# Kernel optimization log

Measured on AMD Instinct MI355X. Metric: run time of the kernel, lower is better.

The kernel has to match this reference:

```python
import jax, jax.numpy as jnp
import numpy as np

DIM = 768; NH = 8; G = 14; N = G * G + 1; B = 64; PD = DIM // 16; HID = 4 * DIM
SCOPES = (1, 4, 7)


def _build_adj(fs, scope):
    # windowed adjacency on an fs x fs grid, padded with an always-on ACM (class) token
    idx = np.arange(fs)
    ii, jj = np.meshgrid(idx, idx, indexing='ij')
    ri, rj = ii.ravel(), jj.ravel()
    a = ((np.abs(ri[:, None] - ri[None, :]) <= scope) & (np.abs(rj[:, None] - rj[None, :]) <= scope)).astype(np.float32)
    out = np.ones((fs * fs + 1, fs * fs + 1), np.float32)
    out[1:, 1:] = a
    return out


def _prior_adj():
    # loop=0 -> loop1=loop2=0, repeat = NH//4; heads get [adj1,adj1,adj2,adj2,adj3,adj3,ones,ones]
    rep = NH // 4
    mats = [_build_adj(G, s) for s in SCOPES] + [np.ones((N, N), np.float32)]
    return np.stack([m for m in mats for _ in range(rep)], 0)


def _rel_idx():
    coords = np.stack(np.meshgrid(np.arange(G), np.arange(G), indexing='ij')).reshape(2, -1)
    rel = (coords[:, :, None] - coords[:, None, :]).transpose(1, 2, 0).copy()
    rel[..., 0] += G - 1
    rel[..., 1] += G - 1
    rel[..., 0] *= 2 * G - 1
    idx = rel.sum(-1)
    out = np.full((N, N), (2 * G - 1) ** 2 + 1, np.int32)
    out[1:, 1:] = idx
    return out


def _biases():
    r = np.arange(-G, G + 1)  # arange(1-(G+1), G+1)
    g = np.stack(np.meshgrid(r, r, indexing='ij')).reshape(2, -1).T
    return g.astype(np.float32)  # ((2G+1)^2, 2)


def setup_inputs():
    key = jax.random.key(0)
    ks = iter(jax.random.split(key, 32))
    rn = lambda *s: jax.random.normal(next(ks), s, jnp.float32) * 0.02
    return dict(
        x=jax.random.normal(next(ks), (B, N, DIM), jnp.float32),
        norm1_w=jnp.ones(DIM), norm1_b=jnp.zeros(DIM),
        qkv_w=rn(3 * DIM, DIM),
        scale=10.0 * jnp.ones((NH, 1, 1)),
        pp_w=rn(PD, 2), pp_b=jnp.zeros(PD),
        ln1_w=jnp.ones(PD), ln1_b=jnp.zeros(PD), fcp1_w=rn(PD, PD), fcp1_b=jnp.zeros(PD),
        ln2_w=jnp.ones(PD), ln2_b=jnp.zeros(PD), fcp2_w=rn(PD, PD), fcp2_b=jnp.zeros(PD),
        ln3_w=jnp.ones(PD), ln3_b=jnp.zeros(PD), fcp3_w=rn(NH, PD), fcp3_b=jnp.zeros(NH),
        pre_w=rn(NH, NH) + jnp.eye(NH), post_w=rn(NH, NH) + jnp.eye(NH),
        proj_w=rn(DIM, DIM), proj_b=jnp.zeros(DIM),
        norm2_w=jnp.ones(DIM), norm2_b=jnp.zeros(DIM),
        m1_w=rn(HID, DIM), m1_b=jnp.zeros(HID),
        m2_w=rn(DIM, HID), m2_b=jnp.zeros(DIM),
        prior_adj=jnp.asarray(_prior_adj()),
        biases=jnp.asarray(_biases()),
        rel_idx=jnp.asarray(_rel_idx()),
    )


def _ln(x, w, b, eps=1e-5):
    m = x.mean(-1, keepdims=True)
    v = ((x - m) ** 2).mean(-1, keepdims=True)
    return (x - m) / jnp.sqrt(v + eps) * w + b


def _l2n(x, eps=1e-12):
    return x / jnp.maximum(jnp.linalg.norm(x, axis=-1, keepdims=True), eps)


def reference(x, norm1_w, norm1_b, qkv_w, scale, pp_w, pp_b, ln1_w, ln1_b, fcp1_w, fcp1_b, ln2_w, ln2_b, fcp2_w, fcp2_b, ln3_w, ln3_b, fcp3_w, fcp3_b, pre_w, post_w, proj_w, proj_b, norm2_w, norm2_b, m1_w, m1_b, m2_w, m2_b, prior_adj, biases, rel_idx):
    Bq, Nq, C = x.shape
    d = C // NH
    h = _ln(x, norm1_w, norm1_b)
    qkv = (h @ qkv_w.T).reshape(Bq, Nq, 3, NH, d).transpose(2, 0, 3, 1, 4)
    q, k, v = qkv[0], qkv[1], qkv[2]  # each (B, NH, N, d)
    attn = jnp.einsum('bhnd,bhmd->bhnm', _l2n(q), _l2n(k)) * jnp.minimum(scale, 100.0)[None]
    p = biases @ pp_w.T + pp_b
    p = jax.nn.relu(_ln(p, ln1_w, ln1_b)) @ fcp1_w.T + fcp1_b
    p = jax.nn.relu(_ln(p, ln2_w, ln2_b)) @ fcp2_w.T + fcp2_b
    p = jax.nn.relu(_ln(p, ln3_w, ln3_b)) @ fcp3_w.T + fcp3_b  # (841, NH)
    rpb = p[rel_idx]  # (N, N, NH)
    attn = attn + rpb.transpose(2, 0, 1)[None]
    attn = jnp.einsum('oh,bhnm->bonm', pre_w, attn)  # 1x1 conv over heads (pre-softmax)
    attn = jnp.where(prior_adj[None] > 0, attn, -1e9)
    attn = jax.nn.softmax(attn, axis=-1)
    attn = jnp.einsum('oh,bhnm->bonm', post_w, attn)  # 1x1 conv over heads (post-softmax)
    out = jnp.einsum('bhnm,bhmd->bhnd', attn, v).transpose(0, 2, 1, 3).reshape(Bq, Nq, C)
    x = x + (out @ proj_w.T + proj_b)
    h2 = _ln(x, norm2_w, norm2_b)
    h2 = jax.nn.gelu(h2 @ m1_w.T + m1_b, approximate=False) @ m2_w.T + m2_b
    return x + h2
```

## Files before the change

kernel.cpp:

```cpp
#include <hip/hip_runtime.h>
#include <hip/hip_bf16.h>
#include <math.h>

typedef __hip_bfloat16 bf16;
typedef __attribute__((ext_vector_type(8))) short bf16x8;
typedef __attribute__((ext_vector_type(4))) float f32x4;

__device__ __forceinline__ float b2f(bf16 x){ return __bfloat162float(x); }
__device__ __forceinline__ bf16  f2b(float x){ return __float2bfloat16(x); }

__device__ __forceinline__ void gld16(const bf16* g, bf16* l){
    __builtin_amdgcn_global_load_lds(
        (const __attribute__((address_space(1))) unsigned int*)g,
        (__attribute__((address_space(3))) unsigned int*)l, 16, 0, 0);
}

#define NTOK 197
#define NBATCH 64
#define NHEAD 8
#define DHEAD 96
#define DIMC 768
#define NROWS (NBATCH * NTOK)
#define VTS 224
#define SMS 208
#define MHALF 6304

#define OFF_P   0ull
#define OFF_W   32768ull
#define SZ_QKVW 3538944ull
#define SZ_PRJW 1179648ull
#define SZ_M1W  4718592ull
#define SZ_M2W  4718592ull
#define OFF_H   14188544ull
#define SZ_H    19365888ull
#define OFF_Q   33554432ull
#define OFF_K   52920320ull
#define OFF_V   72286208ull

__global__ __launch_bounds__(256) void w_cvt_all(
    const float* __restrict__ s0, const float* __restrict__ s1,
    const float* __restrict__ s2, const float* __restrict__ s3, bf16* __restrict__ d)
{
    int i = blockIdx.x*256 + threadIdx.x;
    const float* s; int off;
    if (i < 442368){ s=s0; off=i; }
    else if (i < 589824){ s=s1; off=i-442368; }
    else if (i < 1179648){ s=s2; off=i-589824; }
    else { s=s3; off=i-1179648; }
    float4 v = ((const float4*)s)[off];
    bf16 t[4] = {f2b(v.x), f2b(v.y), f2b(v.z), f2b(v.w)};
    ((ushort4*)d)[i] = *(ushort4*)t;
}

__global__ __launch_bounds__(256) void vt_pad(bf16* __restrict__ vt){
    int i = blockIdx.x*256 + threadIdx.x;
    if (i < 49152*27){
        int r = i/27, c = 197 + (i - r*27);
        vt[(size_t)r*VTS + c] = f2b(0.f);
    }
}

__global__ __launch_bounds__(64) void pos_mlp(
    const float* __restrict__ biases, const float* __restrict__ pp_w, const float* __restrict__ pp_b,
    const float* __restrict__ ln1w, const float* __restrict__ ln1b,
    const float* __restrict__ f1w,  const float* __restrict__ f1b,
    const float* __restrict__ ln2w, const float* __restrict__ ln2b,
    const float* __restrict__ f2w,  const float* __restrict__ f2b,
    const float* __restrict__ ln3w, const float* __restrict__ ln3b,
    const float* __restrict__ f3w,  const float* __restrict__ f3b,
    float* __restrict__ pout)
{
    const int row = blockIdx.x, j = threadIdx.x;
    __shared__ float va[48], vb[48];
    float b0 = biases[row*2], b1 = biases[row*2+1];
    if (j < 48) va[j] = b0*pp_w[j*2] + b1*pp_w[j*2+1] + pp_b[j];
    __syncthreads();
    {   float s=0.f, s2=0.f;
        for (int i=0;i<48;i++){ float t=va[i]; s+=t; s2+=t*t; }
        float mean=s*(1.f/48.f), var=s2*(1.f/48.f)-mean*mean, inv=rsqrtf(var+1e-5f);
        float r=0.f;
        if (j < 48){
            r = f1b[j];
            for (int i=0;i<48;i++){
                float t = fmaxf((va[i]-mean)*inv*ln1w[i] + ln1b[i], 0.f);
                r += t * f1w[j*48+i];
            }
        }
        __syncthreads();
        if (j < 48) vb[j] = r;
    }
    __syncthreads();
    {   float s=0.f, s2=0.f;
        for (int i=0;i<48;i++){ float t=vb[i]; s+=t; s2+=t*t; }
        float mean=s*(1.f/48.f), var=s2*(1.f/48.f)-mean*mean, inv=rsqrtf(var+1e-5f);
        float r=0.f;
        if (j < 48){
            r = f2b[j];
            for (int i=0;i<48;i++){
                float t = fmaxf((vb[i]-mean)*inv*ln2w[i] + ln2b[i], 0.f);
                r += t * f2w[j*48+i];
            }
        }
        __syncthreads();
        if (j < 48) va[j] = r;
    }
    __syncthreads();
    {   float s=0.f, s2=0.f;
        for (int i=0;i<48;i++){ float t=va[i]; s+=t; s2+=t*t; }
        float mean=s*(1.f/48.f), var=s2*(1.f/48.f)-mean*mean, inv=rsqrtf(var+1e-5f);
        if (j < 8){
            float r = f3b[j];
            for (int i=0;i<48;i++){
                float t = fmaxf((va[i]-mean)*inv*ln3w[i] + ln3b[i], 0.f);
                r += t * f3w[j*48+i];
            }
            pout[row*8+j] = r;
        }
    }
}

__device__ __forceinline__ float ldf(const bf16& x){ return __bfloat162float(x); }
__device__ __forceinline__ float ldf(const float& x){ return x; }

template<typename TIN>
__global__ __launch_bounds__(256) void ln768(
    const TIN* __restrict__ x, const float* __restrict__ w, const float* __restrict__ b,
    bf16* __restrict__ out)
{
    const int row = blockIdx.x, tid = threadIdx.x;
    const int wv = tid >> 6, ln = tid & 63;
    __shared__ float rs[4], rs2[4];
    const TIN* xr = x + (size_t)row * DIMC;
    float v0 = ldf(xr[tid]), v1 = ldf(xr[tid+256]), v2 = ldf(xr[tid+512]);
    float s = v0+v1+v2, s2 = v0*v0+v1*v1+v2*v2;
    #pragma unroll
    for (int off=32; off; off>>=1){ s += __shfl_xor(s,off,64); s2 += __shfl_xor(s2,off,64); }
    if (ln == 0){ rs[wv]=s; rs2[wv]=s2; }
    __syncthreads();
    s = rs[0]+rs[1]+rs[2]+rs[3]; s2 = rs2[0]+rs2[1]+rs2[2]+rs2[3];
    float mean = s*(1.f/768.f), var = s2*(1.f/768.f) - mean*mean;
    float inv = rsqrtf(var + 1e-5f);
    size_t base = (size_t)row * DIMC;
    out[base+tid]     = f2b((v0-mean)*inv*w[tid]     + b[tid]);
    out[base+tid+256] = f2b((v1-mean)*inv*w[tid+256] + b[tid+256]);
    out[base+tid+512] = f2b((v2-mean)*inv*w[tid+512] + b[tid+512]);
}

__global__ __launch_bounds__(256) void l2norm_qk(bf16* __restrict__ q, bf16* __restrict__ k)
{
    const int wv = threadIdx.x >> 6, ln = threadIdx.x & 63;
    const size_t NR = (size_t)NBATCH*NHEAD*NTOK;
    size_t row = (size_t)blockIdx.x * 4 + wv;
    bf16* ptr = (row < NR) ? (q + row*DHEAD) : (k + (row-NR)*DHEAD);
    float x0 = b2f(ptr[ln]);
    float x1 = (ln < 32) ? b2f(ptr[64+ln]) : 0.f;
    float ss = x0*x0 + x1*x1;
    #pragma unroll
    for (int off=32; off; off>>=1) ss += __shfl_xor(ss,off,64);
    float inv = 1.f / fmaxf(sqrtf(ss), 1e-12f);
    ptr[ln] = f2b(x0*inv);
    if (ln < 32) ptr[64+ln] = f2b(x1*inv);
}

__global__ __launch_bounds__(256) void attn_mfma(
    const bf16* __restrict__ q, const bf16* __restrict__ k, const bf16* __restrict__ vt,
    const float* __restrict__ p, const float* __restrict__ scale,
    const float* __restrict__ pre_w, const float* __restrict__ post_w,
    bf16* __restrict__ ao)
{
    const int id = blockIdx.x;
    const int r8 = id & 7, t8 = id >> 3;
    const int bx = t8 % 25, b = r8 + 8*(t8/25);
    const int n0 = bx*8;
    const int tid = threadIdx.x, wv = tid>>6, ln = tid&63;
    const int fr = ln&15, fq = ln>>4;
    __shared__ float S[NHEAD*8*SMS];
    __shared__ float s_pre[64], s_post[64], s_sc[8];
    bf16* Sb = (bf16*)S;
    if (tid < 64){ s_pre[tid]=pre_w[tid]; s_post[tid]=post_w[tid]; }
    if (tid < 8)  s_sc[tid] = fminf(scale[tid], 100.f);

    #pragma unroll
    for (int hh=0; hh<2; hh++){
        const int h = wv + hh*4;
        int qr = n0 + fr; if (qr > 196) qr = 196;
        const bf16* qrow = q + ((size_t)(b*NHEAD+h)*NTOK + qr)*DHEAD + fq*8;
        bf16x8 a0 = *(const bf16x8*)(qrow);
        bf16x8 a1 = *(const bf16x8*)(qrow+32);
        bf16x8 a2 = *(const bf16x8*)(qrow+64);
        const bf16* kb0 = k + (size_t)(b*NHEAD+h)*NTOK*DHEAD + fq*8;
        const bf16* kr = kb0 + (size_t)fr*DHEAD;
        bf16x8 kv0 = *(const bf16x8*)(kr);
        bf16x8 kv1 = *(const bf16x8*)(kr+32);
        bf16x8 kv2 = *(const bf16x8*)(kr+64);
        for (int mt=0; mt<13; mt++){
            bf16x8 c0=kv0, c1=kv1, c2=kv2;
            if (mt < 12){
                int nr = (mt+1)*16+fr; if (nr>196) nr=196;
                const bf16* kn = kb0 + (size_t)nr*DHEAD;
                kv0 = *(const bf16x8*)(kn);
                kv1 = *(const bf16x8*)(kn+32);
                kv2 = *(const bf16x8*)(kn+64);
            }
            f32x4 acc = {};
            acc = __builtin_amdgcn_mfma_f32_16x16x32_bf16(a0, c0, acc,0,0,0);
            acc = __builtin_amdgcn_mfma_f32_16x16x32_bf16(a1, c1, acc,0,0,0);
            acc = __builtin_amdgcn_mfma_f32_16x16x32_bf16(a2, c2, acc,0,0,0);
            if (fq < 2){
                #pragma unroll
                for (int i=0;i<4;i++)
                    S[(h*8 + fq*4+i)*SMS + mt*16+fr] = acc[i];
            }
        }
    }
    __syncthreads();

    const int sco[8] = {1,1,4,4,7,7,1000,1000};
    for (int c=tid; c<8*SMS; c+=256){
        int nq = c/SMS, m = c - nq*SMS;
        if (m >= 197){
            #pragma unroll
            for (int o=0;o<8;o++) S[(o*8+nq)*SMS+m] = -1e9f;
            continue;
        }
        int n = n0+nq; if (n > 196) n = 196;
        bool always = (n==0) || (m==0);
        int ri=0, ci=0, rj=0, cj=0;
        if (!always){
            ri=(n-1)/14; ci=(n-1)-ri*14;
            rj=(m-1)/14; cj=(m-1)-rj*14;
        }
        int dr = ri-rj; if (dr<0) dr=-dr;
        int dc = ci-cj; if (dc<0) dc=-dc;
        int idx = always ? 730 : (ri-rj+13)*27 + (ci-cj+13);
        const float* pv = p + idx*8;
        float sh[8];
        #pragma unroll
        for (int h=0;h<8;h++) sh[h] = S[(h*8+nq)*SMS+m]*s_sc[h] + pv[h];
        float ov[8];
        #pragma unroll
        for (int o=0;o<8;o++){
            float v=0.f;
            #pragma unroll
            for (int hh2=0;hh2<8;hh2++) v += s_pre[o*8+hh2]*sh[hh2];
            bool on = always || (dr<=sco[o] && dc<=sco[o]);
            ov[o] = on ? v : -1e9f;
        }
        #pragma unroll
        for (int o=0;o<8;o++) S[(o*8+nq)*SMS+m] = ov[o];
    }
    __syncthreads();

    for (int r = wv*16; r < wv*16+16; r++){
        float* row = &S[r*SMS];
        float mx = -3e38f;
        for (int m=ln; m<SMS; m+=64) mx = fmaxf(mx, row[m]);
        #pragma unroll
        for (int off=32; off; off>>=1) mx = fmaxf(mx, __shfl_xor(mx,off,64));
        float sum = 0.f;
        for (int m=ln; m<SMS; m+=64){ float e=__expf(row[m]-mx); row[m]=e; sum+=e; }
        #pragma unroll
        for (int off=32; off; off>>=1) sum += __shfl_xor(sum,off,64);
        float inv = 1.f/sum;
        for (int m=ln; m<SMS; m+=64) row[m] *= inv;
    }
    __syncthreads();

    float ov[7][8];
    #pragma unroll
    for (int kk=0; kk<7; kk++){
        int c = tid + kk*256;
        if (c < 8*197){
            int nq = c/197, m = c - nq*197;
            float ph[8];
            #pragma unroll
            for (int o=0;o<8;o++) ph[o] = S[(o*8+nq)*SMS+m];
            #pragma unroll
            for (int o2=0;o2<8;o2++){
                float v=0.f;
                #pragma unroll
                for (int o=0;o<8;o++) v += s_post[o2*8+o]*ph[o];
                ov[kk][o2]=v;
            }
        }
    }
    __syncthreads();
    #pragma unroll
    for (int kk=0; kk<7; kk++){
        int c = tid + kk*256;
        if (c < 8*197){
            int nq = c/197, m = c - nq*197;
            #pragma unroll
            for (int o=0;o<8;o++) Sb[(o*8+nq)*416 + m] = f2b(ov[kk][o]);
        }
    }
    for (int i=tid; i<64*27; i+=256){
        int r = i/27, mm = 197 + (i - (i/27)*27);
        Sb[r*416 + mm] = f2b(0.f);
    }
    __syncthreads();

    const int frA = fr & 7;
    #pragma unroll
    for (int hh=0; hh<2; hh++){
        const int h = wv + hh*4;
        const bf16* vbase = vt + (size_t)(b*NHEAD+h)*DHEAD*VTS;
        for (int dt=0; dt<6; dt++){
            f32x4 acc = {};
            #pragma unroll
            for (int ks=0; ks<7; ks++){
                const bf16* ap = Sb + (h*8+frA)*416 + ks*32 + fq*8;
                const bf16* bp = vbase + (size_t)(dt*16+fr)*VTS + ks*32 + fq*8;
                acc = __builtin_amdgcn_mfma_f32_16x16x32_bf16(*(const bf16x8*)ap, *(const bf16x8*)bp, acc,0,0,0);
            }
            #pragma unroll
            for (int i=0;i<4;i++){
                int nq = fq*4+i, n = n0+nq;
                if (nq < 8 && n < NTOK)
                    ao[((size_t)b*NTOK+n)*DIMC + h*DHEAD + dt*16+fr] = f2b(acc[i]);
            }
        }
    }
}

enum { EPI_QKV=0, EPI_X1=1, EPI_GELU=2, EPI_OUT=3 };

template<int EPI>
__global__ __launch_bounds__(256) void gemm128(
    const bf16* __restrict__ A, int lda, int M,
    const bf16* __restrict__ B, int ldb,
    int K,
    const float* __restrict__ bias,
    const float* __restrict__ resid_f,
    const bf16* __restrict__ resid_b,
    float* __restrict__ dst_f,
    bf16* __restrict__ dst_b, int lddb,
    int row_off,
    bf16* __restrict__ qo, bf16* __restrict__ ko, bf16* __restrict__ vto)
{
    __shared__ bf16 As[128*32];
    __shared__ bf16 Bs[128*32];
    const int tid = threadIdx.x;
    const int wv = tid >> 6, ln = tid & 63;
    const int fr = ln & 15, fq = ln >> 4;
    const int wr = (wv & 1)*64, wc = (wv >> 1)*64;
    const int m0 = blockIdx.y*128, n0 = blockIdx.x*128;
    const int lnrow = ln >> 2, lncol = (ln & 3)*8;
    f32x4 acc[4][4] = {};
    for (int k0=0; k0<K; k0+=32){
        #pragma unroll
        for (int c=0;c<2;c++){
            int rA = m0 + (c*4+wv)*16 + lnrow;
            if (rA >= M) rA = M-1;
            gld16(A + (size_t)rA*lda + k0 + lncol, &As[(c*4+wv)*16*32]);
            int rB = n0 + (c*4+wv)*16 + lnrow;
            gld16(B + (size_t)rB*ldb + k0 + lncol, &Bs[(c*4+wv)*16*32]);
        }
        __syncthreads();
        bf16x8 af[4], bfv[4];
        #pragma unroll
        for (int i=0;i<4;i++){
            af[i]  = *(const bf16x8*)&As[(wr + i*16 + fr)*32 + fq*8];
            bfv[i] = *(const bf16x8*)&Bs[(wc + i*16 + fr)*32 + fq*8];
        }
        #pragma unroll
        for (int mi=0;mi<4;mi++)
            #pragma unroll
            for (int ni=0;ni<4;ni++)
                acc[mi][ni] = __builtin_amdgcn_mfma_f32_16x16x32_bf16(af[mi], bfv[ni], acc[mi][ni],0,0,0);
        __syncthreads();
    }
    #pragma unroll
    for (int mi=0;mi<4;mi++){
        #pragma unroll
        for (int ni=0;ni<4;ni++){
            #pragma unroll
            for (int i=0;i<4;i++){
                int row = m0 + wr + mi*16 + fq*4 + i;
                int col = n0 + wc + ni*16 + fr;
                if (row >= M) continue;
                float val = acc[mi][ni][i];
                if constexpr (EPI == EPI_QKV){
                    int which = col/768, rem = col - which*768;
                    int hh = rem/96, di = rem - hh*96;
                    int bb = row/NTOK, nn = row - bb*NTOK;
                    if (which == 0)      qo[(((size_t)bb*NHEAD+hh)*NTOK+nn)*DHEAD + di] = f2b(val);
                    else if (which == 1) ko[(((size_t)bb*NHEAD+hh)*NTOK+nn)*DHEAD + di] = f2b(val);
                    else                 vto[(((size_t)bb*NHEAD+hh)*DHEAD+di)*VTS + nn] = f2b(val);
                } else if constexpr (EPI == EPI_X1){
                    dst_b[(size_t)row*DIMC + col] = f2b(val + bias[col] + resid_f[(size_t)row*DIMC + col]);
                } else if constexpr (EPI == EPI_GELU){
                    float t = val + bias[col];
                    t = 0.5f*t*(1.f + erff(t*0.70710678118654752f));
                    dst_b[(size_t)row*lddb + col] = f2b(t);
                } else {
                    size_t g = (size_t)(row + row_off)*DIMC + col;
                    dst_f[g] = val + bias[col] + b2f(resid_b[g]);
                }
            }
        }
    }
}

extern "C" void kernel_launch(void* const* d_in, const int* in_sizes, int n_in,
                              void* d_out, int out_size, void* d_ws, size_t ws_size,
                              hipStream_t stream)
{
    const float* x        = (const float*)d_in[0];
    const float* norm1_w  = (const float*)d_in[1];
    const float* norm1_b  = (const float*)d_in[2];
    const float* qkv_w    = (const float*)d_in[3];
    const float* scale    = (const float*)d_in[4];
    const float* pp_w     = (const float*)d_in[5];
    const float* pp_b     = (const float*)d_in[6];
    const float* ln1_w    = (const float*)d_in[7];
    const float* ln1_b    = (const float*)d_in[8];
    const float* fcp1_w   = (const float*)d_in[9];
    const float* fcp1_b   = (const float*)d_in[10];
    const float* ln2_w    = (const float*)d_in[11];
    const float* ln2_b    = (const float*)d_in[12];
    const float* fcp2_w   = (const float*)d_in[13];
    const float* fcp2_b   = (const float*)d_in[14];
    const float* ln3_w    = (const float*)d_in[15];
    const float* ln3_b    = (const float*)d_in[16];
    const float* fcp3_w   = (const float*)d_in[17];
    const float* fcp3_b   = (const float*)d_in[18];
    const float* pre_w    = (const float*)d_in[19];
    const float* post_w   = (const float*)d_in[20];
    const float* proj_w   = (const float*)d_in[21];
    const float* proj_b   = (const float*)d_in[22];
    const float* nrm2_w   = (const float*)d_in[23];
    const float* nrm2_b   = (const float*)d_in[24];
    const float* m1_w     = (const float*)d_in[25];
    const float* m1_b     = (const float*)d_in[26];
    const float* m2_w     = (const float*)d_in[27];
    const float* m2_b     = (const float*)d_in[28];
    const float* biases   = (const float*)d_in[30];
    float* out = (float*)d_out;

    char* ws = (char*)d_ws;
    float* p      = (float*)(ws + OFF_P);
    bf16*  qkvw_b = (bf16*)(ws + OFF_W);
    bf16*  prjw_b = (bf16*)(ws + OFF_W + SZ_QKVW);
    bf16*  m1w_b  = (bf16*)(ws + OFF_W + SZ_QKVW + SZ_PRJW);
    bf16*  m2w_b  = (bf16*)(ws + OFF_W + SZ_QKVW + SZ_PRJW + SZ_M1W);
    bf16*  h   = (bf16*)(ws + OFF_H);
    bf16*  qb  = (bf16*)(ws + OFF_Q);
    bf16*  kb  = (bf16*)(ws + OFF_K);
    bf16*  vt  = (bf16*)(ws + OFF_V);
    bf16*  ao  = (bf16*)(ws + OFF_H);
    bf16*  x1b = (bf16*)(ws + OFF_V);
    bf16*  h2  = (bf16*)(ws + OFF_K);
    bf16*  mid = (bf16*)(ws + OFF_H);

    w_cvt_all<<<6912, 256, 0, stream>>>(qkv_w, proj_w, m1_w, m2_w, qkvw_b);
    pos_mlp<<<841, 64, 0, stream>>>(biases, pp_w, pp_b, ln1_w, ln1_b, fcp1_w, fcp1_b,
                                    ln2_w, ln2_b, fcp2_w, fcp2_b, ln3_w, ln3_b, fcp3_w, fcp3_b, p);
    ln768<float><<<NROWS, 256, 0, stream>>>(x, norm1_w, norm1_b, h);
    gemm128<EPI_QKV><<<dim3(18, 99), 256, 0, stream>>>(
        h, DIMC, NROWS, qkvw_b, DIMC, DIMC, nullptr, nullptr, nullptr, nullptr,
        nullptr, 0, 0, qb, kb, vt);
    vt_pad<<<5184, 256, 0, stream>>>(vt);
    l2norm_qk<<<(NBATCH*NHEAD*NTOK*2)/4, 256, 0, stream>>>(qb, kb);
    attn_mfma<<<1600, 256, 0, stream>>>(qb, kb, vt, p, scale, pre_w, post_w, ao);
    gemm128<EPI_X1><<<dim3(6, 99), 256, 0, stream>>>(
        ao, DIMC, NROWS, prjw_b, DIMC, DIMC, proj_b, x, nullptr, nullptr,
        x1b, 0, 0, nullptr, nullptr, nullptr);
    ln768<bf16><<<NROWS, 256, 0, stream>>>(x1b, nrm2_w, nrm2_b, h2);
    for (int c=0; c<2; c++){
        const int r0 = c*MHALF;
        gemm128<EPI_GELU><<<dim3(24, 50), 256, 0, stream>>>(
            h2 + (size_t)r0*DIMC, DIMC, MHALF, m1w_b, DIMC, DIMC, m1_b,
            nullptr, nullptr, nullptr, mid, 3072, 0, nullptr, nullptr, nullptr);
        gemm128<EPI_OUT><<<dim3(6, 50), 256, 0, stream>>>(
            mid, 3072, MHALF, m2w_b, 3072, 3072, m2_b,
            nullptr, x1b, out, nullptr, 0, r0, nullptr, nullptr, nullptr);
    }
    (void)in_sizes; (void)n_in; (void)out_size; (void)ws_size;
}
```

Measured before the change: 891.3 us.

## Deepen GEMM K-step to 64, fuse V padding into QKV epilogue, pad attention LDS rows

The GEMM main loop now loads two 32-wide K slices per iteration into doubled LDS buffers, which halves the number of barrier pairs per tile. The separate vt_pad launch is removed, and the QKV epilogue zeroes the V^T padding columns alongside the V writes. The attention kernel's score-row stride changes from 208 to 228 floats and the bf16 stride from 416 to 456, likely to reduce LDS bank conflicts, while the loops keep a 224 logical width. In exchange, the GEMM uses more LDS and the attention kernel's shared footprint grows, which may reduce occupancy.

```diff
diff --git a/kernel.cpp b/kernel.cpp
--- a/kernel.cpp
+++ b/kernel.cpp
@@ -22,7 +22,7 @@
 #define DIMC 768
 #define NROWS (NBATCH * NTOK)
 #define VTS 224
-#define SMS 208
+#define SMS 228
 #define MHALF 6304
 
 #define OFF_P   0ull
@@ -50,14 +50,6 @@
     float4 v = ((const float4*)s)[off];
     bf16 t[4] = {f2b(v.x), f2b(v.y), f2b(v.z), f2b(v.w)};
     ((ushort4*)d)[i] = *(ushort4*)t;
-}
-
-__global__ __launch_bounds__(256) void vt_pad(bf16* __restrict__ vt){
-    int i = blockIdx.x*256 + threadIdx.x;
-    if (i < 49152*27){
-        int r = i/27, c = 197 + (i - r*27);
-        vt[(size_t)r*VTS + c] = f2b(0.f);
-    }
 }
 
 __global__ __launch_bounds__(64) void pos_mlp(
@@ -216,8 +208,8 @@
     __syncthreads();
 
     const int sco[8] = {1,1,4,4,7,7,1000,1000};
-    for (int c=tid; c<8*SMS; c+=256){
-        int nq = c/SMS, m = c - nq*SMS;
+    for (int c=tid; c<8*224; c+=256){
+        int nq = c/224, m = c - nq*224;
         if (m >= 197){
             #pragma unroll
             for (int o=0;o<8;o++) S[(o*8+nq)*SMS+m] = -1e9f;
@@ -254,15 +246,15 @@
     for (int r = wv*16; r < wv*16+16; r++){
         float* row = &S[r*SMS];
         float mx = -3e38f;
-        for (int m=ln; m<SMS; m+=64) mx = fmaxf(mx, row[m]);
+        for (int m=ln; m<224; m+=64) mx = fmaxf(mx, row[m]);
         #pragma unroll
         for (int off=32; off; off>>=1) mx = fmaxf(mx, __shfl_xor(mx,off,64));
         float sum = 0.f;
-        for (int m=ln; m<SMS; m+=64){ float e=__expf(row[m]-mx); row[m]=e; sum+=e; }
+        for (int m=ln; m<224; m+=64){ float e=__expf(row[m]-mx); row[m]=e; sum+=e; }
         #pragma unroll
         for (int off=32; off; off>>=1) sum += __shfl_xor(sum,off,64);
         float inv = 1.f/sum;
-        for (int m=ln; m<SMS; m+=64) row[m] *= inv;
+        for (int m=ln; m<224; m+=64) row[m] *= inv;
     }
     __syncthreads();
 
@@ -291,12 +283,12 @@
         if (c < 8*197){
             int nq = c/197, m = c - nq*197;
             #pragma unroll
-            for (int o=0;o<8;o++) Sb[(o*8+nq)*416 + m] = f2b(ov[kk][o]);
+            for (int o=0;o<8;o++) Sb[(o*8+nq)*456 + m] = f2b(ov[kk][o]);
         }
     }
     for (int i=tid; i<64*27; i+=256){
         int r = i/27, mm = 197 + (i - (i/27)*27);
-        Sb[r*416 + mm] = f2b(0.f);
+        Sb[r*456 + mm] = f2b(0.f);
     }
     __syncthreads();
 
@@ -309,7 +301,7 @@
             f32x4 acc = {};
             #pragma unroll
             for (int ks=0; ks<7; ks++){
-                const bf16* ap = Sb + (h*8+frA)*416 + ks*32 + fq*8;
+                const bf16* ap = Sb + (h*8+frA)*456 + ks*32 + fq*8;
                 const bf16* bp = vbase + (size_t)(dt*16+fr)*VTS + ks*32 + fq*8;
                 acc = __builtin_amdgcn_mfma_f32_16x16x32_bf16(*(const bf16x8*)ap, *(const bf16x8*)bp, acc,0,0,0);
             }
@@ -338,8 +330,8 @@
     int row_off,
     bf16* __restrict__ qo, bf16* __restrict__ ko, bf16* __restrict__ vto)
 {
-    __shared__ bf16 As[128*32];
-    __shared__ bf16 Bs[128*32];
+    __shared__ bf16 As[2*128*32];
+    __shared__ bf16 Bs[2*128*32];
     const int tid = threadIdx.x;
     const int wv = tid >> 6, ln = tid & 63;
     const int fr = ln & 15, fq = ln >> 4;
@@ -347,27 +339,33 @@
     const int m0 = blockIdx.y*128, n0 = blockIdx.x*128;
     const int lnrow = ln >> 2, lncol = (ln & 3)*8;
     f32x4 acc[4][4] = {};
-    for (int k0=0; k0<K; k0+=32){
-        #pragma unroll
-        for (int c=0;c<2;c++){
-            int rA = m0 + (c*4+wv)*16 + lnrow;
-            if (rA >= M) rA = M-1;
-            gld16(A + (size_t)rA*lda + k0 + lncol, &As[(c*4+wv)*16*32]);
-            int rB = n0 + (c*4+wv)*16 + lnrow;
-            gld16(B + (size_t)rB*ldb + k0 + lncol, &Bs[(c*4+wv)*16*32]);
+    for (int k0=0; k0<K; k0+=64){
+        #pragma unroll
+        for (int t=0;t<2;t++){
+            #pragma unroll
+            for (int c=0;c<2;c++){
+                int rA = m0 + (c*4+wv)*16 + lnrow;
+                if (rA >= M) rA = M-1;
+                gld16(A + (size_t)rA*lda + k0 + t*32 + lncol, &As[t*4096 + (c*4+wv)*16*32]);
+                int rB = n0 + (c*4+wv)*16 + lnrow;
+                gld16(B + (size_t)rB*ldb + k0 + t*32 + lncol, &Bs[t*4096 + (c*4+wv)*16*32]);
+            }
         }
         __syncthreads();
-        bf16x8 af[4], bfv[4];
-        #pragma unroll
-        for (int i=0;i<4;i++){
-            af[i]  = *(const bf16x8*)&As[(wr + i*16 + fr)*32 + fq*8];
-            bfv[i] = *(const bf16x8*)&Bs[(wc + i*16 + fr)*32 + fq*8];
-        }
-        #pragma unroll
-        for (int mi=0;mi<4;mi++)
-            #pragma unroll
-            for (int ni=0;ni<4;ni++)
-                acc[mi][ni] = __builtin_amdgcn_mfma_f32_16x16x32_bf16(af[mi], bfv[ni], acc[mi][ni],0,0,0);
+        #pragma unroll
+        for (int t=0;t<2;t++){
+            bf16x8 af[4], bfv[4];
+            #pragma unroll
+            for (int i=0;i<4;i++){
+                af[i]  = *(const bf16x8*)&As[t*4096 + (wr + i*16 + fr)*32 + fq*8];
+                bfv[i] = *(const bf16x8*)&Bs[t*4096 + (wc + i*16 + fr)*32 + fq*8];
+            }
+            #pragma unroll
+            for (int mi=0;mi<4;mi++)
+                #pragma unroll
+                for (int ni=0;ni<4;ni++)
+                    acc[mi][ni] = __builtin_amdgcn_mfma_f32_16x16x32_bf16(af[mi], bfv[ni], acc[mi][ni],0,0,0);
+        }
         __syncthreads();
     }
     #pragma unroll
@@ -386,7 +384,11 @@
                     int bb = row/NTOK, nn = row - bb*NTOK;
                     if (which == 0)      qo[(((size_t)bb*NHEAD+hh)*NTOK+nn)*DHEAD + di] = f2b(val);
                     else if (which == 1) ko[(((size_t)bb*NHEAD+hh)*NTOK+nn)*DHEAD + di] = f2b(val);
-                    else                 vto[(((size_t)bb*NHEAD+hh)*DHEAD+di)*VTS + nn] = f2b(val);
+                    else {
+                        vto[(((size_t)bb*NHEAD+hh)*DHEAD+di)*VTS + nn] = f2b(val);
+                        if (nn < VTS - NTOK)
+                            vto[(((size_t)bb*NHEAD+hh)*DHEAD+di)*VTS + NTOK + nn] = f2b(0.f);
+                    }
                 } else if constexpr (EPI == EPI_X1){
                     dst_b[(size_t)row*DIMC + col] = f2b(val + bias[col] + resid_f[(size_t)row*DIMC + col]);
                 } else if constexpr (EPI == EPI_GELU){
@@ -460,7 +462,6 @@
     gemm128<EPI_QKV><<<dim3(18, 99), 256, 0, stream>>>(
         h, DIMC, NROWS, qkvw_b, DIMC, DIMC, nullptr, nullptr, nullptr, nullptr,
         nullptr, 0, 0, qb, kb, vt);
-    vt_pad<<<5184, 256, 0, stream>>>(vt);
     l2norm_qk<<<(NBATCH*NHEAD*NTOK*2)/4, 256, 0, stream>>>(qb, kb);
     attn_mfma<<<1600, 256, 0, stream>>>(qb, kb, vt, p, scale, pre_w, post_w, ao);
     gemm128<EPI_X1><<<dim3(6, 99), 256, 0, stream>>>(
```

New measurement: 846.4 us. 1.05x faster.
